# Optimization experiments

Measured on AMD Instinct MI355X. Metric: run time of the kernel, lower is better.

The kernel has to match this reference:

```python
import jax, jax.numpy as jnp
import numpy as np

EPS = 1e-08


def setup_inputs() -> dict:
    key = jax.random.key(0)
    k1, k2, k3, k4 = jax.random.split(key, 4)
    src_len, bsz, d = 2048, 32, 1024
    inp = {
        "input": jax.random.normal(k1, (bsz, d), dtype=jnp.float32),
        "source_hids": jax.random.normal(k2, (src_len, bsz, d), dtype=jnp.float32),
        "encoder_padding_mask": jnp.zeros((src_len, bsz), dtype=bool),
        "W_in": jax.random.normal(k3, (d, d), dtype=jnp.float32) * (d ** -0.5),
        "W_out": jax.random.normal(k4, (d, 2 * d), dtype=jnp.float32) * ((2 * d) ** -0.5),
    }
    return inp


def reference(input, source_hids, encoder_padding_mask, W_in, W_out):
    # ProductEnergyLayer (scale=False): energy = sum_d source_hids * (input @ W_in^T)
    x = input @ W_in.T  # [bsz, ctx]
    energy = jnp.einsum("sbd,bd->sb", source_hids, x)  # [src_len, bsz]
    energy = jnp.where(encoder_padding_mask, -1e9, energy)

    # p_choose = sigmoid(monotonic energy)
    p = jax.nn.sigmoid(energy)  # [src_len, bsz]

    # exclusive cumprod of (1 - p) along src_len
    one_minus_p = 1.0 - p
    ones_row = jnp.ones_like(p[:1])
    cumprod_1mp = jnp.cumprod(jnp.concatenate([ones_row, one_minus_p[:-1]], axis=0), axis=0)

    denominator = jnp.clip(cumprod_1mp, EPS, 1.0)

    # previous_attention defaults to one-hot at position 0
    prev_attn = jnp.zeros_like(p).at[0].set(1.0)

    # alpha = p * cumprod(1-p) * cumsum(prev / cumprod(1-p))
    alpha = p * cumprod_1mp * jnp.cumsum(prev_attn / denominator, axis=0)

    # monotonic_type == 'hard' -> beta = alpha
    beta = alpha

    # weighted context and output projection
    weighted_context = jnp.einsum("sbd,sb->bd", source_hids, beta)  # [bsz, ctx]
    output = jnp.tanh(jnp.concatenate([weighted_context, input], axis=1) @ W_out.T)
    return output, beta, alpha
```

## Files before the change

### kernel.cpp

```cpp
#include <hip/hip_runtime.h>
#include <hip/hip_bf16.h>
#include <math.h>


#define SRC_LEN 2048
#define BSZ     32
#define DIM     1024
#define CH      64
#define TAIL4   ((SRC_LEN - CH) * BSZ / 4)

__global__ __launch_bounds__(256) void k_xproj(const float* __restrict__ input,
                                               const float* __restrict__ W,
                                               float* __restrict__ x) {
    int wid  = blockIdx.x * 4 + (threadIdx.x >> 6);
    int lane = threadIdx.x & 63;
    int b    = wid >> 6;
    int i0   = (wid & 63) * 16;
    const float4* inp = (const float4*)(input + (size_t)b * DIM);
    float4 in[4];
    #pragma unroll
    for (int k = 0; k < 4; ++k) in[k] = inp[lane + 64 * k];
    #pragma unroll 4
    for (int i = 0; i < 16; ++i) {
        const float4* wr = (const float4*)(W + (size_t)(i0 + i) * DIM);
        float acc = 0.f;
        #pragma unroll
        for (int k = 0; k < 4; ++k) {
            float4 wv = wr[lane + 64 * k];
            acc += wv.x * in[k].x + wv.y * in[k].y + wv.z * in[k].z + wv.w * in[k].w;
        }
        #pragma unroll
        for (int off = 32; off; off >>= 1) acc += __shfl_down(acc, off);
        if (lane == 0) x[(size_t)b * DIM + i0 + i] = acc;
    }
}

__global__ __launch_bounds__(256) void k_energy_fill(const float* __restrict__ src,
                                                     const float* __restrict__ x,
                                                     float* __restrict__ energy,
                                                     float* __restrict__ beta_out,
                                                     float* __restrict__ alpha_out) {
    int bid = blockIdx.x;
    if (bid < 512) {
        int wid  = bid * 4 + (threadIdx.x >> 6);
        int lane = threadIdx.x & 63;
        int s = wid >> 5, b = wid & (BSZ - 1);
        const float4* row = (const float4*)(src + ((size_t)s * BSZ + b) * DIM);
        const float4* xr  = (const float4*)(x + (size_t)b * DIM);
        float acc = 0.f;
        #pragma unroll
        for (int k = 0; k < 4; ++k) {
            float4 v = row[lane + 64 * k];
            float4 c = xr[lane + 64 * k];
            acc += v.x * c.x + v.y * c.y + v.z * c.z + v.w * c.w;
        }
        #pragma unroll
        for (int off = 32; off; off >>= 1) acc += __shfl_down(acc, off);
        if (lane == 0) energy[(size_t)s * BSZ + b] = acc;
    } else {
        int i = (bid - 512) * 256 + threadIdx.x;
        if (i < TAIL4) {
            float4 z = {0.f, 0.f, 0.f, 0.f};
            ((float4*)(beta_out  + (size_t)CH * BSZ))[i] = z;
            ((float4*)(alpha_out + (size_t)CH * BSZ))[i] = z;
        }
    }
}

__global__ __launch_bounds__(1024) void k_scan_wc(const float* __restrict__ src,
                                                  const float* __restrict__ x,
                                                  const unsigned char* __restrict__ mask,
                                                  const float* __restrict__ energy,
                                                  float* __restrict__ beta_out,
                                                  float* __restrict__ alpha_out,
                                                  float* __restrict__ wc) {
    int b = blockIdx.x;
    int t = threadIdx.x;
    int w = t >> 6, lane = t & 63;
    __shared__ float pb[CH];
    __shared__ int   snz;
    __shared__ float cstate;
    __shared__ float red[16];
    __shared__ float crun, bcur;
    __shared__ __align__(16) float xs[DIM];

    if (w == 0) {
        float ev = energy[(size_t)lane * BSZ + b];
        if (mask[(size_t)lane * BSZ + b]) ev = -1e9f;
        float p  = 1.0f / (1.0f + expf(-ev));
        float om = 1.0f - p;
        float prod = om;
        #pragma unroll
        for (int off = 1; off < 64; off <<= 1) {
            float o = __shfl_up(prod, off);
            if (lane >= off) prod *= o;
        }
        float excl = __shfl_up(prod, 1);
        if (lane == 0) excl = 1.0f;
        float a = p * excl;
        beta_out[(size_t)lane * BSZ + b]  = a;
        alpha_out[(size_t)lane * BSZ + b] = a;
        pb[lane] = a;
        unsigned long long nz = __ballot(a != 0.0f);
        if (lane == 0) snz = (nz == 0ULL) ? 0 : (64 - __builtin_clzll(nz));
        if (lane == 63) cstate = prod;
    }
    __syncthreads();

    float acc = 0.f;
    int smax = snz;
    for (int s = 0; s < smax; ++s) {
        float wgt = pb[s];
        if (wgt != 0.0f) acc += wgt * src[((size_t)s * BSZ + b) * DIM + t];
    }

    if (cstate != 0.0f) {
        for (int i = t; i < DIM; i += 1024) xs[i] = x[(size_t)b * DIM + i];
        if (t == 0) crun = cstate;
        __syncthreads();
        for (int s = CH; s < SRC_LEN; ++s) {
            float v = src[((size_t)s * BSZ + b) * DIM + t];
            float part = v * xs[t];
            #pragma unroll
            for (int off = 32; off; off >>= 1) part += __shfl_down(part, off);
            if (lane == 0) red[w] = part;
            __syncthreads();
            if (t == 0) {
                float ev = 0.f;
                #pragma unroll
                for (int i = 0; i < 16; ++i) ev += red[i];
                if (mask[(size_t)s * BSZ + b]) ev = -1e9f;
                float p = 1.0f / (1.0f + expf(-ev));
                float a = p * crun;
                beta_out[(size_t)s * BSZ + b]  = a;
                alpha_out[(size_t)s * BSZ + b] = a;
                bcur = a;
                crun = crun * (1.0f - p);
            }
            __syncthreads();
            acc += bcur * v;
            if (crun == 0.0f) break;
        }
    }

    wc[(size_t)b * DIM + t] = acc;
}

__global__ __launch_bounds__(256) void k_out(const float* __restrict__ wc,
                                             const float* __restrict__ input,
                                             const float* __restrict__ W,
                                             float* __restrict__ out) {
    int wid  = blockIdx.x * 4 + (threadIdx.x >> 6);
    int lane = threadIdx.x & 63;
    int bp   = wid >> 6;
    int o0   = (wid & 63) * 16;
    int b0 = bp * 2, b1 = bp * 2 + 1;
    const float4* wc0 = (const float4*)(wc + (size_t)b0 * DIM);
    const float4* wc1 = (const float4*)(wc + (size_t)b1 * DIM);
    const float4* in0 = (const float4*)(input + (size_t)b0 * DIM);
    const float4* in1 = (const float4*)(input + (size_t)b1 * DIM);
    float4 c0[4], c1[4], u0[4], u1[4];
    #pragma unroll
    for (int k = 0; k < 4; ++k) {
        c0[k] = wc0[lane + 64 * k]; c1[k] = wc1[lane + 64 * k];
        u0[k] = in0[lane + 64 * k]; u1[k] = in1[lane + 64 * k];
    }
    #pragma unroll 2
    for (int i = 0; i < 16; ++i) {
        const float4* wr = (const float4*)(W + (size_t)(o0 + i) * 2 * DIM);
        float a0 = 0.f, a1 = 0.f;
        #pragma unroll
        for (int k = 0; k < 4; ++k) {
            float4 wv = wr[lane + 64 * k];
            a0 += wv.x * c0[k].x + wv.y * c0[k].y + wv.z * c0[k].z + wv.w * c0[k].w;
            a1 += wv.x * c1[k].x + wv.y * c1[k].y + wv.z * c1[k].z + wv.w * c1[k].w;
        }
        #pragma unroll
        for (int k = 0; k < 4; ++k) {
            float4 wv = wr[256 + lane + 64 * k];
            a0 += wv.x * u0[k].x + wv.y * u0[k].y + wv.z * u0[k].z + wv.w * u0[k].w;
            a1 += wv.x * u1[k].x + wv.y * u1[k].y + wv.z * u1[k].z + wv.w * u1[k].w;
        }
        #pragma unroll
        for (int off = 32; off; off >>= 1) {
            a0 += __shfl_down(a0, off);
            a1 += __shfl_down(a1, off);
        }
        if (lane == 0) {
            out[(size_t)b0 * DIM + o0 + i] = tanhf(a0);
            out[(size_t)b1 * DIM + o0 + i] = tanhf(a1);
        }
    }
}

extern "C" void kernel_launch(void* const* d_in, const int* in_sizes, int n_in,
                              void* d_out, int out_size, void* d_ws, size_t ws_size,
                              hipStream_t stream) {
    const float* input = (const float*)d_in[0];
    const float* src   = (const float*)d_in[1];
    const unsigned char* mask = (const unsigned char*)d_in[2];
    const float* W_in  = (const float*)d_in[3];
    const float* W_out = (const float*)d_in[4];

    float* out_proj  = (float*)d_out;
    float* beta_out  = out_proj + BSZ * DIM;
    float* alpha_out = beta_out + SRC_LEN * BSZ;

    float* ws = (float*)d_ws;
    float* x      = ws;
    float* wc     = x + BSZ * DIM;
    float* energy = wc + BSZ * DIM;

    k_xproj<<<512, 256, 0, stream>>>(input, W_in, x);
    k_energy_fill<<<512 + 64, 256, 0, stream>>>(src, x, energy, beta_out, alpha_out);
    k_scan_wc<<<BSZ, 1024, 0, stream>>>(src, x, mask, energy, beta_out, alpha_out, wc);
    k_out<<<256, 256, 0, stream>>>(wc, input, W_out, out_proj);
}
```

Measured before the change: 31.77 us.

## Fuse energy into scan kernel, merge fill with xproj, batch GEMV rows

Computes the first-chunk energies inside the per-batch attention kernel using x staged in shared memory, which drops the separate energy kernel and its global round trip. The zero-fill of the beta/alpha tail moves into the x-projection kernel. Both GEMV kernels now process four batch rows per wave so each weight row is reused four times, which halves the block count for the output projection. Together these remove one launch and cut weight traffic, at the cost of more registers per thread and energy work concentrated on only 32 blocks.

```diff
diff --git a/kernel.cpp b/kernel.cpp
--- a/kernel.cpp
+++ b/kernel.cpp
@@ -8,84 +8,103 @@
 #define DIM     1024
 #define CH      64
 #define TAIL4   ((SRC_LEN - CH) * BSZ / 4)
-
-__global__ __launch_bounds__(256) void k_xproj(const float* __restrict__ input,
-                                               const float* __restrict__ W,
-                                               float* __restrict__ x) {
-    int wid  = blockIdx.x * 4 + (threadIdx.x >> 6);
-    int lane = threadIdx.x & 63;
-    int b    = wid >> 6;
-    int i0   = (wid & 63) * 16;
-    const float4* inp = (const float4*)(input + (size_t)b * DIM);
-    float4 in[4];
-    #pragma unroll
-    for (int k = 0; k < 4; ++k) in[k] = inp[lane + 64 * k];
-    #pragma unroll 4
-    for (int i = 0; i < 16; ++i) {
-        const float4* wr = (const float4*)(W + (size_t)(i0 + i) * DIM);
-        float acc = 0.f;
-        #pragma unroll
-        for (int k = 0; k < 4; ++k) {
-            float4 wv = wr[lane + 64 * k];
-            acc += wv.x * in[k].x + wv.y * in[k].y + wv.z * in[k].z + wv.w * in[k].w;
-        }
-        #pragma unroll
-        for (int off = 32; off; off >>= 1) acc += __shfl_down(acc, off);
-        if (lane == 0) x[(size_t)b * DIM + i0 + i] = acc;
-    }
-}
-
-__global__ __launch_bounds__(256) void k_energy_fill(const float* __restrict__ src,
-                                                     const float* __restrict__ x,
-                                                     float* __restrict__ energy,
-                                                     float* __restrict__ beta_out,
-                                                     float* __restrict__ alpha_out) {
+#define XPB     128
+#define FILLB   (TAIL4 / 256)
+
+__global__ __launch_bounds__(256) void k_xproj_fill(const float* __restrict__ input,
+                                                    const float* __restrict__ W,
+                                                    float* __restrict__ x,
+                                                    float* __restrict__ beta_out,
+                                                    float* __restrict__ alpha_out) {
     int bid = blockIdx.x;
-    if (bid < 512) {
-        int wid  = bid * 4 + (threadIdx.x >> 6);
-        int lane = threadIdx.x & 63;
-        int s = wid >> 5, b = wid & (BSZ - 1);
-        const float4* row = (const float4*)(src + ((size_t)s * BSZ + b) * DIM);
-        const float4* xr  = (const float4*)(x + (size_t)b * DIM);
-        float acc = 0.f;
-        #pragma unroll
-        for (int k = 0; k < 4; ++k) {
-            float4 v = row[lane + 64 * k];
-            float4 c = xr[lane + 64 * k];
-            acc += v.x * c.x + v.y * c.y + v.z * c.z + v.w * c.w;
-        }
-        #pragma unroll
-        for (int off = 32; off; off >>= 1) acc += __shfl_down(acc, off);
-        if (lane == 0) energy[(size_t)s * BSZ + b] = acc;
+    int t = threadIdx.x;
+    if (bid < XPB) {
+        int wid  = bid * 4 + (t >> 6);
+        int lane = t & 63;
+        int bq   = wid >> 6;
+        int i0   = (wid & 63) * 16;
+        float4 in[4][4];
+        #pragma unroll
+        for (int q = 0; q < 4; ++q) {
+            const float4* inp = (const float4*)(input + (size_t)(bq * 4 + q) * DIM);
+            #pragma unroll
+            for (int k = 0; k < 4; ++k) in[q][k] = inp[lane + 64 * k];
+        }
+        #pragma unroll 2
+        for (int i = 0; i < 16; ++i) {
+            const float4* wr = (const float4*)(W + (size_t)(i0 + i) * DIM);
+            float4 wv[4];
+            #pragma unroll
+            for (int k = 0; k < 4; ++k) wv[k] = wr[lane + 64 * k];
+            float acc[4] = {0.f, 0.f, 0.f, 0.f};
+            #pragma unroll
+            for (int k = 0; k < 4; ++k) {
+                #pragma unroll
+                for (int q = 0; q < 4; ++q)
+                    acc[q] += wv[k].x * in[q][k].x + wv[k].y * in[q][k].y
+                            + wv[k].z * in[q][k].z + wv[k].w * in[q][k].w;
+            }
+            #pragma unroll
+            for (int off = 32; off; off >>= 1) {
+                acc[0] += __shfl_down(acc[0], off);
+                acc[1] += __shfl_down(acc[1], off);
+                acc[2] += __shfl_down(acc[2], off);
+                acc[3] += __shfl_down(acc[3], off);
+            }
+            if (lane == 0) {
+                #pragma unroll
+                for (int q = 0; q < 4; ++q)
+                    x[(size_t)(bq * 4 + q) * DIM + i0 + i] = acc[q];
+            }
+        }
     } else {
-        int i = (bid - 512) * 256 + threadIdx.x;
-        if (i < TAIL4) {
-            float4 z = {0.f, 0.f, 0.f, 0.f};
-            ((float4*)(beta_out  + (size_t)CH * BSZ))[i] = z;
-            ((float4*)(alpha_out + (size_t)CH * BSZ))[i] = z;
-        }
-    }
-}
-
-__global__ __launch_bounds__(1024) void k_scan_wc(const float* __restrict__ src,
-                                                  const float* __restrict__ x,
-                                                  const unsigned char* __restrict__ mask,
-                                                  const float* __restrict__ energy,
-                                                  float* __restrict__ beta_out,
-                                                  float* __restrict__ alpha_out,
-                                                  float* __restrict__ wc) {
+        int i = (bid - XPB) * 256 + t;
+        float4 z = {0.f, 0.f, 0.f, 0.f};
+        ((float4*)(beta_out  + (size_t)CH * BSZ))[i] = z;
+        ((float4*)(alpha_out + (size_t)CH * BSZ))[i] = z;
+    }
+}
+
+__global__ __launch_bounds__(1024) void k_attn(const float* __restrict__ src,
+                                               const float* __restrict__ x,
+                                               const unsigned char* __restrict__ mask,
+                                               float* __restrict__ beta_out,
+                                               float* __restrict__ alpha_out,
+                                               float* __restrict__ wc) {
     int b = blockIdx.x;
     int t = threadIdx.x;
     int w = t >> 6, lane = t & 63;
+    __shared__ __align__(16) float xs[DIM];
+    __shared__ float e[CH];
     __shared__ float pb[CH];
     __shared__ int   snz;
     __shared__ float cstate;
     __shared__ float red[16];
     __shared__ float crun, bcur;
-    __shared__ __align__(16) float xs[DIM];
+
+    for (int i = t; i < DIM; i += 1024) xs[i] = x[(size_t)b * DIM + i];
+    __syncthreads();
+
+    const float4* x4 = (const float4*)xs;
+    #pragma unroll
+    for (int r = 0; r < 4; ++r) {
+        int s = w + 16 * r;
+        const float4* row = (const float4*)(src + ((size_t)s * BSZ + b) * DIM);
+        float acc = 0.f;
+        #pragma unroll
+        for (int it = 0; it < 4; ++it) {
+            float4 v = row[it * 64 + lane];
+            float4 c = x4[it * 64 + lane];
+            acc += v.x * c.x + v.y * c.y + v.z * c.z + v.w * c.w;
+        }
+        #pragma unroll
+        for (int off = 32; off; off >>= 1) acc += __shfl_down(acc, off);
+        if (lane == 0) e[s] = acc;
+    }
+    __syncthreads();
 
     if (w == 0) {
-        float ev = energy[(size_t)lane * BSZ + b];
+        float ev = e[lane];
         if (mask[(size_t)lane * BSZ + b]) ev = -1e9f;
         float p  = 1.0f / (1.0f + expf(-ev));
         float om = 1.0f - p;
@@ -115,7 +134,6 @@
     }
 
     if (cstate != 0.0f) {
-        for (int i = t; i < DIM; i += 1024) xs[i] = x[(size_t)b * DIM + i];
         if (t == 0) crun = cstate;
         __syncthreads();
         for (int s = CH; s < SRC_LEN; ++s) {
@@ -152,43 +170,49 @@
                                              float* __restrict__ out) {
     int wid  = blockIdx.x * 4 + (threadIdx.x >> 6);
     int lane = threadIdx.x & 63;
-    int bp   = wid >> 6;
+    int bq   = wid >> 6;
     int o0   = (wid & 63) * 16;
-    int b0 = bp * 2, b1 = bp * 2 + 1;
-    const float4* wc0 = (const float4*)(wc + (size_t)b0 * DIM);
-    const float4* wc1 = (const float4*)(wc + (size_t)b1 * DIM);
-    const float4* in0 = (const float4*)(input + (size_t)b0 * DIM);
-    const float4* in1 = (const float4*)(input + (size_t)b1 * DIM);
-    float4 c0[4], c1[4], u0[4], u1[4];
+    float4 c[4][4], u[4][4];
     #pragma unroll
-    for (int k = 0; k < 4; ++k) {
-        c0[k] = wc0[lane + 64 * k]; c1[k] = wc1[lane + 64 * k];
-        u0[k] = in0[lane + 64 * k]; u1[k] = in1[lane + 64 * k];
-    }
-    #pragma unroll 2
+    for (int q = 0; q < 4; ++q) {
+        const float4* wcp = (const float4*)(wc    + (size_t)(bq * 4 + q) * DIM);
+        const float4* inp = (const float4*)(input + (size_t)(bq * 4 + q) * DIM);
+        #pragma unroll
+        for (int k = 0; k < 4; ++k) {
+            c[q][k] = wcp[lane + 64 * k];
+            u[q][k] = inp[lane + 64 * k];
+        }
+    }
     for (int i = 0; i < 16; ++i) {
         const float4* wr = (const float4*)(W + (size_t)(o0 + i) * 2 * DIM);
-        float a0 = 0.f, a1 = 0.f;
+        float acc[4] = {0.f, 0.f, 0.f, 0.f};
         #pragma unroll
         for (int k = 0; k < 4; ++k) {
             float4 wv = wr[lane + 64 * k];
-            a0 += wv.x * c0[k].x + wv.y * c0[k].y + wv.z * c0[k].z + wv.w * c0[k].w;
-            a1 += wv.x * c1[k].x + wv.y * c1[k].y + wv.z * c1[k].z + wv.w * c1[k].w;
+            #pragma unroll
+            for (int q = 0; q < 4; ++q)
+                acc[q] += wv.x * c[q][k].x + wv.y * c[q][k].y
+                        + wv.z * c[q][k].z + wv.w * c[q][k].w;
         }
         #pragma unroll
         for (int k = 0; k < 4; ++k) {
             float4 wv = wr[256 + lane + 64 * k];
-            a0 += wv.x * u0[k].x + wv.y * u0[k].y + wv.z * u0[k].z + wv.w * u0[k].w;
-            a1 += wv.x * u1[k].x + wv.y * u1[k].y + wv.z * u1[k].z + wv.w * u1[k].w;
+            #pragma unroll
+            for (int q = 0; q < 4; ++q)
+                acc[q] += wv.x * u[q][k].x + wv.y * u[q][k].y
+                        + wv.z * u[q][k].z + wv.w * u[q][k].w;
         }
         #pragma unroll
         for (int off = 32; off; off >>= 1) {
-            a0 += __shfl_down(a0, off);
-            a1 += __shfl_down(a1, off);
+            acc[0] += __shfl_down(acc[0], off);
+            acc[1] += __shfl_down(acc[1], off);
+            acc[2] += __shfl_down(acc[2], off);
+            acc[3] += __shfl_down(acc[3], off);
         }
         if (lane == 0) {
-            out[(size_t)b0 * DIM + o0 + i] = tanhf(a0);
-            out[(size_t)b1 * DIM + o0 + i] = tanhf(a1);
+            #pragma unroll
+            for (int q = 0; q < 4; ++q)
+                out[(size_t)(bq * 4 + q) * DIM + o0 + i] = tanhf(acc[q]);
         }
     }
 }
@@ -207,12 +231,10 @@
     float* alpha_out = beta_out + SRC_LEN * BSZ;
 
     float* ws = (float*)d_ws;
-    float* x      = ws;
-    float* wc     = x + BSZ * DIM;
-    float* energy = wc + BSZ * DIM;
-
-    k_xproj<<<512, 256, 0, stream>>>(input, W_in, x);
-    k_energy_fill<<<512 + 64, 256, 0, stream>>>(src, x, energy, beta_out, alpha_out);
-    k_scan_wc<<<BSZ, 1024, 0, stream>>>(src, x, mask, energy, beta_out, alpha_out, wc);
-    k_out<<<256, 256, 0, stream>>>(wc, input, W_out, out_proj);
-}
+    float* x  = ws;
+    float* wc = x + BSZ * DIM;
+
+    k_xproj_fill<<<XPB + FILLB, 256, 0, stream>>>(input, W_in, x, beta_out, alpha_out);
+    k_attn<<<BSZ, 1024, 0, stream>>>(src, x, mask, beta_out, alpha_out, wc);
+    k_out<<<128, 256, 0, stream>>>(wc, input, W_out, out_proj);
+}
```

After: 56.50 us. 77.8% more time.
